# Kernel tuning notes

Measured on AMD Instinct MI355X. Metric: run time of the kernel, lower is better.

The kernel has to match this reference:

```python
import jax, jax.numpy as jnp
import numpy as np


def _conv2d_same(x, w):
    # x: [B,Cin,H,W], w: [Cout,Cin,3,3], stride 1, padding 1
    return jax.lax.conv_general_dilated(
        x, w, window_strides=(1, 1), padding=[(1, 1), (1, 1)],
        dimension_numbers=('NCHW', 'OIHW', 'NCHW'))


def _unfold3x3(x):
    # torch.nn.Unfold(kernel_size=3, padding=1, stride=1):
    # output [B, C*9, H*W], channel-major then kernel row-major ordering.
    b, c, h, w = x.shape
    xp = jnp.pad(x, ((0, 0), (0, 0), (1, 1), (1, 1)))
    patches = jnp.stack(
        [xp[:, :, i:i + h, j:j + w] for i in range(3) for j in range(3)],
        axis=2)  # [B, C, 9, H, W]
    return patches.reshape(b, c * 9, h * w)


def setup_inputs() -> dict:
    key = jax.random.key(0)
    ks = jax.random.split(key, 6)
    B, C, H, W = 16, 64, 128, 128
    R = 16
    return {
        'x': jax.random.normal(ks[0], (B, C, H, W), dtype=jnp.float32),
        'weight': jax.random.normal(ks[1], (C, C, 3, 3), dtype=jnp.float32) * 0.1,
        'se_w1': jax.random.normal(ks[2], (16, C, 3, 3), dtype=jnp.float32) * 0.1,
        'se_w2': jax.random.normal(ks[3], (1, 16, 3, 3), dtype=jnp.float32) * 0.1,
        'fc_w1': jax.random.normal(ks[4], (C // R, C), dtype=jnp.float32) * 0.1,
        'fc_w2': jax.random.normal(ks[5], (9 * C, C // R), dtype=jnp.float32) * 0.1,
    }


def reference(x, weight, se_w1, se_w2, fc_w1, fc_w2):
    b, c, h, w = x.shape
    # channel attention: global avg pool -> fc -> sigmoid, y: [B, C*9]
    y = x.mean(axis=(2, 3))                                   # [B, C]
    y = jax.nn.relu(y @ fc_w1.T)                              # [B, C//r]
    y = jax.nn.sigmoid(y @ fc_w2.T)                           # [B, 9C]
    # spatial attention A: [B, 1, H, W]
    A = jax.nn.sigmoid(_conv2d_same(jax.nn.relu(_conv2d_same(x, se_w1)), se_w2))
    out_unfold = _unfold3x3(x)                                # [B, C*9, HW]
    out_unfold = out_unfold * A.reshape(b, 1, h * w) * y[:, :, None]
    wf = weight.reshape(c, c * 9)                             # [Cout, C*9]
    out = jnp.einsum('bkl,ok->bol', out_unfold, wf)           # [B, Cout, HW]
    return out.reshape(b, c, h, w)
```

## Files before the change

### kernel.cpp

```cpp
#include <hip/hip_runtime.h>
#include <hip/hip_bf16.h>
#include <math.h>

#define B_  16
#define C_  64
#define H_  128
#define W_  128
#define HW_ (H_ * W_)
#define CR_ 4
#define K9C (9 * C_)
#define TW  130
#define FBS 36
#define STG_W 36
#define STG_H 12
#define MIDOFF (STG_H * STG_W * 128)
#define MIDS 18
#define WTB 8192
#define W2OFF (MIDOFF + 3 * WTB)
#define LDSZ  (W2OFF + 144 * 4)

typedef float f32x4 __attribute__((ext_vector_type(4)));
typedef __bf16 bf16x8 __attribute__((ext_vector_type(8)));

static __device__ __forceinline__ unsigned short f2us(float f) {
    __bf16 h = (__bf16)f;
    return __builtin_bit_cast(unsigned short, h);
}

static __device__ __forceinline__ int swz64(int blk) {
    int xcd = blk & 7, i = blk >> 3;
    return ((i >> 6) << 9) + (xcd << 6) + (i & 63);
}

__global__ void k_tr(const float* __restrict__ x, unsigned short* __restrict__ t,
                     float* __restrict__ y0p) {
    int blk = blockIdx.x;
    int b = blk >> 7, y = blk & 127;
    __shared__ unsigned short lds[C_ * TW];
    int tid = threadIdx.x;
    for (int i = tid; i < C_ * 32; i += 256) {
        int c = i >> 5, xq = i & 31;
        float4 v = *(const float4*)(x + (((size_t)(b * C_ + c)) << 14) + (y << 7) + (xq << 2));
        unsigned int p0 = f2us(v.x) | ((unsigned int)f2us(v.y) << 16);
        unsigned int p1 = f2us(v.z) | ((unsigned int)f2us(v.w) << 16);
        *(unsigned int*)&lds[c * TW + (xq << 2)]     = p0;
        *(unsigned int*)&lds[c * TW + (xq << 2) + 2] = p1;
        float s4 = v.x + v.y + v.z + v.w;
        s4 += __shfl_down(s4, 16, 32);
        s4 += __shfl_down(s4, 8, 32);
        s4 += __shfl_down(s4, 4, 32);
        s4 += __shfl_down(s4, 2, 32);
        s4 += __shfl_down(s4, 1, 32);
        if ((tid & 31) == 0) y0p[(((b << 7) + y) << 6) + c] = s4;
    }
    __syncthreads();
    size_t rowbase = ((size_t)(b * TW + y + 1)) * TW * C_;
    for (int j = tid; j < 128 * 16; j += 256) {
        int px = j >> 4, g = j & 15;
        unsigned short a0 = lds[(4 * g + 0) * TW + px];
        unsigned short a1 = lds[(4 * g + 1) * TW + px];
        unsigned short a2 = lds[(4 * g + 2) * TW + px];
        unsigned short a3 = lds[(4 * g + 3) * TW + px];
        uint2 wv;
        wv.x = a0 | ((unsigned int)a1 << 16);
        wv.y = a2 | ((unsigned int)a3 << 16);
        *(uint2*)(t + rowbase + (size_t)(px + 1) * C_ + (g << 2)) = wv;
    }
    if (tid < 16) {
        int px = (tid < 8) ? 0 : (TW - 1);
        int ch = tid & 7;
        uint4 z = {0, 0, 0, 0};
        *(uint4*)(t + rowbase + (size_t)px * C_ + ch * 8) = z;
    }
    if (y == 0) {
        size_t base = (size_t)b * TW * TW * C_;
        uint4 z = {0, 0, 0, 0};
        for (int i = tid; i < TW * C_ / 8; i += 256)
            *(uint4*)(t + base + (size_t)i * 8) = z;
    }
    if (y == 127) {
        size_t base = ((size_t)(b * TW + TW - 1)) * TW * C_;
        uint4 z = {0, 0, 0, 0};
        for (int i = tid; i < TW * C_ / 8; i += 256)
            *(uint4*)(t + base + (size_t)i * 8) = z;
    }
}

__global__ void k_attwt(const float* __restrict__ y0p,
                        const float* __restrict__ fc_w1,
                        const float* __restrict__ fc_w2,
                        const float* __restrict__ weight,
                        const float* __restrict__ se_w1,
                        unsigned short* __restrict__ w_t,
                        unsigned short* __restrict__ w1t) {
    int blk = blockIdx.x;
    int b = blk >> 2, mt = blk & 3;
    __shared__ float sy0[C_];
    __shared__ float sh[CR_];
    __shared__ float ssy[K9C];
    __shared__ float sw[16 * 576];
    int tid = threadIdx.x;
    if (blk == 0) {
        for (int i = tid; i < 9 * 16 * C_; i += 256) {
            int tap = i >> 10, o = (i >> 6) & 15, c = i & 63;
            w1t[i] = f2us(se_w1[(o * C_ + c) * 9 + tap]);
        }
    }
    if (tid < C_) {
        float s = 0.f;
        const float* pp = y0p + ((size_t)b << 13) + tid;
        for (int y = 0; y < 128; ++y) s += pp[y << 6];
        sy0[tid] = s * (1.0f / (float)HW_);
    }
    const float* wsrc = weight + (size_t)(mt * 16) * 576;
    for (int i = tid; i < 16 * 576; i += 256) sw[i] = wsrc[i];
    __syncthreads();
    if (tid < CR_) {
        float s = 0.f;
        for (int c = 0; c < C_; ++c) s = fmaf(fc_w1[tid * C_ + c], sy0[c], s);
        sh[tid] = fmaxf(s, 0.f);
    }
    __syncthreads();
    for (int i = tid; i < K9C; i += 256) {
        float s = 0.f;
        #pragma unroll
        for (int j = 0; j < CR_; ++j) s = fmaf(fc_w2[i * CR_ + j], sh[j], s);
        ssy[i] = 1.f / (1.f + expf(-s));
    }
    __syncthreads();
    unsigned short* wb = w_t + (size_t)b * 9 * C_ * C_;
    for (int ii = tid; ii < 4608; ii += 256) {
        int i = ii << 1;
        int tap = i >> 10, r = i & 1023;
        int half = r >> 9, lane = (r >> 3) & 63, e = r & 7;
        int o = lane & 15;
        int c = half * 32 + ((lane >> 4) << 3) + e;
        float v0 = sw[o * 576 + c * 9 + tap] * ssy[c * 9 + tap];
        float v1 = sw[o * 576 + (c + 1) * 9 + tap] * ssy[(c + 1) * 9 + tap];
        unsigned int pk = f2us(v0) | ((unsigned int)f2us(v1) << 16);
        *(unsigned int*)(wb + ((tap * 4 + mt) * 2 + half) * 512 + lane * 8 + e) = pk;
    }
}

__global__ void __launch_bounds__(512, 4)
k_fused(const unsigned short* __restrict__ t, const unsigned short* __restrict__ w_t,
        const unsigned short* __restrict__ w1t, const float* __restrict__ se_w2,
        float* __restrict__ out) {
    int blk = swz64(blockIdx.x);
    int b = blk >> 6, tile = blk & 63;
    int ty0 = (tile >> 2) << 3, tx0 = (tile & 3) << 5;
    int tid = threadIdx.x, lane = tid & 63, wave = tid >> 6;
    int wy = wave >> 1, wx = wave & 1;
    int n = lane & 15, q = lane >> 4, qc = q << 3;
    __shared__ __align__(16) char smem[LDSZ];
    float* fb  = (float*)smem;
    float* mid = (float*)(smem + MIDOFF);
    float* w2l = (float*)(smem + W2OFF);

    const unsigned short* tbb = t + (size_t)b * TW * TW * C_;
    #pragma unroll
    for (int it = 0; it < 7; ++it) {
        int s = (it << 9) + tid;
        if (s < STG_H * STG_W * 8) {
            int row = s / 288, r = s % 288, px = r >> 3, chp = r & 7;
            int tr = ty0 - 1 + row; tr = tr < 0 ? 0 : (tr > TW - 1 ? TW - 1 : tr);
            int tc = tx0 - 1 + px;  tc = tc < 0 ? 0 : (tc > TW - 1 ? TW - 1 : tc);
            int ch = chp ^ (px & 7);
            __builtin_amdgcn_global_load_lds(
                (const __attribute__((address_space(1))) void*)(tbb + ((size_t)tr * TW + tc) * C_ + (ch << 3)),
                (__attribute__((address_space(3))) void*)(smem + (s << 4)), 16, 0, 0);
        }
    }
    if (tid < 144) w2l[tid] = se_w2[(tid & 15) * 9 + (tid >> 4)];

    const unsigned short* wb = w_t + (size_t)b * 9 * C_ * C_;
    #define STAGE_WT(tp) \
        __builtin_amdgcn_global_load_lds( \
            (const __attribute__((address_space(1))) void*)(wb + (tp) * 4096 + (wave << 9) + (lane << 3)), \
            (__attribute__((address_space(3))) void*)(smem + MIDOFF + ((tp) % 3) * WTB + (wave << 10)), \
            16, 0, 0)
    STAGE_WT(0);
    STAGE_WT(1);
    __syncthreads();

    f32x4 acc[4][2] = {};
    #pragma unroll
    for (int tap = 0; tap < 9; ++tap) {
        if (tap) {
            if (tap < 8) asm volatile("s_waitcnt vmcnt(1)" ::: "memory");
            else         asm volatile("s_waitcnt vmcnt(0)" ::: "memory");
            __builtin_amdgcn_s_barrier();
            __builtin_amdgcn_sched_barrier(0);
        }
        if (tap < 7) STAGE_WT(tap + 2);
        int ki = tap / 3, kj = tap % 3;
        int xl = (wx << 4) + n + kj + 1;
        int xk = xl & 7;
        const char* tapbuf = smem + MIDOFF + (tap % 3) * WTB;
        __builtin_amdgcn_s_setprio(1);
        #pragma unroll
        for (int half = 0; half < 2; ++half) {
            bf16x8 af[4];
            #pragma unroll
            for (int mt = 0; mt < 4; ++mt) {
                uint4 au = *(const uint4*)(tapbuf + (((mt << 1) + half) << 10) + (lane << 4));
                af[mt] = __builtin_bit_cast(bf16x8, au);
            }
            int slot = (((half << 2) + q) ^ xk) << 4;
            #pragma unroll
            for (int j2 = 0; j2 < 2; ++j2) {
                int yl = (wy << 1) + j2 + ki + 1;
                bf16x8 bf = *(const bf16x8*)(smem + (yl * STG_W + xl) * 128 + slot);
                #pragma unroll
                for (int mt = 0; mt < 4; ++mt)
                    acc[mt][j2] = __builtin_amdgcn_mfma_f32_16x16x32_bf16(af[mt], bf, acc[mt][j2], 0, 0, 0);
            }
        }
        __builtin_amdgcn_s_setprio(0);
    }
    #undef STAGE_WT
    __syncthreads();

    int mr[3], mc[3], pp[3];
    bool on[3];
    #pragma unroll
    for (int i = 0; i < 3; ++i) {
        int g = wave + (i << 3);
        on[i] = (g < 22);
        int p = g * 16 + n; if (p > 339) p = 339;
        pp[i] = p; mr[i] = p / 34; mc[i] = p - mr[i] * 34;
    }
    f32x4 a1_0 = {}, a1_1 = {}, a1_2 = {};
    __builtin_amdgcn_s_setprio(1);
    #pragma unroll
    for (int tap = 0; tap < 9; ++tap) {
        int ki = tap / 3, kj = tap % 3;
        uint4 u0 = *(const uint4*)(w1t + (tap * 16 + n) * C_ + qc);
        uint4 u1 = *(const uint4*)(w1t + (tap * 16 + n) * C_ + 32 + qc);
        bf16x8 af0 = __builtin_bit_cast(bf16x8, u0);
        bf16x8 af1 = __builtin_bit_cast(bf16x8, u1);
        #pragma unroll
        for (int i = 0; i < 3; ++i) {
            if (on[i]) {
                int sc = mc[i] + kj;
                int sb = ((mr[i] + ki) * STG_W + sc) * 128;
                bf16x8 b0 = *(const bf16x8*)(smem + sb + ((q ^ (sc & 7)) << 4));
                bf16x8 b1 = *(const bf16x8*)(smem + sb + (((4 + q) ^ (sc & 7)) << 4));
                f32x4 t0 = (i == 0) ? a1_0 : (i == 1) ? a1_1 : a1_2;
                t0 = __builtin_amdgcn_mfma_f32_16x16x32_bf16(af0, b0, t0, 0, 0, 0);
                t0 = __builtin_amdgcn_mfma_f32_16x16x32_bf16(af1, b1, t0, 0, 0, 0);
                if (i == 0) a1_0 = t0; else if (i == 1) a1_1 = t0; else a1_2 = t0;
            }
        }
    }
    __builtin_amdgcn_s_setprio(0);
    #pragma unroll
    for (int i = 0; i < 3; ++i) {
        int g = wave + (i << 3);
        if (on[i] && (g < 21 || n < 4)) {
            int my = ty0 - 1 + mr[i], mx = tx0 - 1 + mc[i];
            bool valid = (my >= 0) && (my < 128) && (mx >= 0) && (mx < 128);
            f32x4 av = (i == 0) ? a1_0 : (i == 1) ? a1_1 : a1_2;
            #pragma unroll
            for (int r = 0; r < 4; ++r)
                mid[pp[i] * MIDS + (q << 2) + r] = valid ? fmaxf(av[r], 0.f) : 0.f;
        }
    }
    __syncthreads();

    float4 wq[9];
    #pragma unroll
    for (int tap = 0; tap < 9; ++tap)
        wq[tap] = *(const float4*)&w2l[tap * 16 + (q << 2)];
    float Av[2];
    #pragma unroll
    for (int j2 = 0; j2 < 2; ++j2) {
        float s = 0.f;
        #pragma unroll
        for (int di = 0; di < 3; ++di) {
            #pragma unroll
            for (int dj = 0; dj < 3; ++dj) {
                int p = ((wy << 1) + j2 + di) * 34 + (wx << 4) + n + dj;
                const float* mp = &mid[p * MIDS + (q << 2)];
                float2 m0 = *(const float2*)mp;
                float2 m1 = *(const float2*)(mp + 2);
                float4 wv = wq[di * 3 + dj];
                s = fmaf(m0.x, wv.x, s);
                s = fmaf(m0.y, wv.y, s);
                s = fmaf(m1.x, wv.z, s);
                s = fmaf(m1.y, wv.w, s);
            }
        }
        s += __shfl_xor(s, 16, 64);
        s += __shfl_xor(s, 32, 64);
        Av[j2] = 1.f / (1.f + expf(-s));
    }

    __syncthreads();
    #pragma unroll
    for (int j2 = 0; j2 < 2; ++j2) {
        #pragma unroll
        for (int mt = 0; mt < 4; ++mt) {
            #pragma unroll
            for (int r = 0; r < 4; ++r) {
                int o = (mt << 4) + (q << 2) + r;
                fb[((j2 << 8) + (wy << 6) + o) * FBS + (wx << 4) + n] = acc[mt][j2][r] * Av[j2];
            }
        }
    }
    __syncthreads();
    #pragma unroll
    for (int it = 0; it < 8; ++it) {
        int s = it * 512 + tid;
        int row = s >> 3, xq = s & 7;
        int j2 = row >> 8, rr = row & 255;
        int wy2 = rr >> 6, o = rr & 63;
        float4 v = *(const float4*)&fb[row * FBS + (xq << 2)];
        *(float4*)(out + (((size_t)(b * C_ + o)) << 14) +
                   ((ty0 + (wy2 << 1) + j2) << 7) + tx0 + (xq << 2)) = v;
    }
}

extern "C" void kernel_launch(void* const* d_in, const int* in_sizes, int n_in,
                              void* d_out, int out_size, void* d_ws, size_t ws_size,
                              hipStream_t stream) {
    const float* x      = (const float*)d_in[0];
    const float* weight = (const float*)d_in[1];
    const float* se_w1  = (const float*)d_in[2];
    const float* se_w2  = (const float*)d_in[3];
    const float* fc_w1  = (const float*)d_in[4];
    const float* fc_w2  = (const float*)d_in[5];
    float* out = (float*)d_out;

    char* ws = (char*)d_ws;
    float* y0p           = (float*)ws;                         ws += (size_t)B_ * H_ * C_ * 4;
    unsigned short* t    = (unsigned short*)ws;                ws += (size_t)B_ * TW * TW * C_ * 2 + 4096;
    unsigned short* w_t  = (unsigned short*)ws;                ws += (size_t)B_ * 9 * C_ * C_ * 2;
    unsigned short* w1t  = (unsigned short*)ws;

    k_tr   <<<B_ * H_, 256, 0, stream>>>(x, t, y0p);
    k_attwt<<<B_ * 4, 256, 0, stream>>>(y0p, fc_w1, fc_w2, weight, se_w1, w_t, w1t);
    k_fused<<<B_ * 64, 512, 0, stream>>>(t, w_t, w1t, se_w2, out);
}
```

Baseline: 175.3 us.

## Pack channel pairs in transpose LDS with XOR swizzle and split attention-weight kernel

The transpose kernel now loads two channels per thread and packs them into 32-bit words in a swizzled LDS tile. This replaces four 16-bit strided reads per output with two 32-bit reads, cutting bank conflicts and LDS instruction count. The attention/weight-prep kernel goes from 64 to 256 blocks: the mean reduction is spread across all threads and the per-tap weight packing is divided into four chunks. Each extra block redundantly recomputes the small FC/sigmoid stage in exchange for more parallelism in this short kernel.

```diff
diff --git a/kernel.cpp b/kernel.cpp
--- a/kernel.cpp
+++ b/kernel.cpp
@@ -36,35 +36,44 @@
                      float* __restrict__ y0p) {
     int blk = blockIdx.x;
     int b = blk >> 7, y = blk & 127;
-    __shared__ unsigned short lds[C_ * TW];
+    __shared__ unsigned int lds2[32 * 128];
     int tid = threadIdx.x;
-    for (int i = tid; i < C_ * 32; i += 256) {
-        int c = i >> 5, xq = i & 31;
-        float4 v = *(const float4*)(x + (((size_t)(b * C_ + c)) << 14) + (y << 7) + (xq << 2));
-        unsigned int p0 = f2us(v.x) | ((unsigned int)f2us(v.y) << 16);
-        unsigned int p1 = f2us(v.z) | ((unsigned int)f2us(v.w) << 16);
-        *(unsigned int*)&lds[c * TW + (xq << 2)]     = p0;
-        *(unsigned int*)&lds[c * TW + (xq << 2) + 2] = p1;
-        float s4 = v.x + v.y + v.z + v.w;
-        s4 += __shfl_down(s4, 16, 32);
-        s4 += __shfl_down(s4, 8, 32);
-        s4 += __shfl_down(s4, 4, 32);
-        s4 += __shfl_down(s4, 2, 32);
-        s4 += __shfl_down(s4, 1, 32);
-        if ((tid & 31) == 0) y0p[(((b << 7) + y) << 6) + c] = s4;
+    int cpair = tid >> 3, q8 = tid & 7;
+    int F = (cpair & 15) << 1;
+    const float* x0 = x + (((size_t)(b * C_ + (cpair << 1))) << 14) + (y << 7);
+    float s0 = 0.f, s1 = 0.f;
+    #pragma unroll
+    for (int k = 0; k < 4; ++k) {
+        int px0 = (q8 + (k << 3)) << 2;
+        float4 v0 = *(const float4*)(x0 + px0);
+        float4 v1 = *(const float4*)(x0 + 16384 + px0);
+        s0 += v0.x + v0.y + v0.z + v0.w;
+        s1 += v1.x + v1.y + v1.z + v1.w;
+        uint2 a, c;
+        a.x = f2us(v0.x) | ((unsigned int)f2us(v1.x) << 16);
+        a.y = f2us(v0.y) | ((unsigned int)f2us(v1.y) << 16);
+        c.x = f2us(v0.z) | ((unsigned int)f2us(v1.z) << 16);
+        c.y = f2us(v0.w) | ((unsigned int)f2us(v1.w) << 16);
+        *(uint2*)&lds2[(cpair << 7) + (px0 ^ F)] = a;
+        *(uint2*)&lds2[(cpair << 7) + ((px0 + 2) ^ F)] = c;
+    }
+    s0 += __shfl_down(s0, 4, 8); s0 += __shfl_down(s0, 2, 8); s0 += __shfl_down(s0, 1, 8);
+    s1 += __shfl_down(s1, 4, 8); s1 += __shfl_down(s1, 2, 8); s1 += __shfl_down(s1, 1, 8);
+    if (q8 == 0) {
+        float2 m = {s0, s1};
+        *(float2*)&y0p[(((b << 7) + y) << 6) + (cpair << 1)] = m;
     }
     __syncthreads();
     size_t rowbase = ((size_t)(b * TW + y + 1)) * TW * C_;
-    for (int j = tid; j < 128 * 16; j += 256) {
-        int px = j >> 4, g = j & 15;
-        unsigned short a0 = lds[(4 * g + 0) * TW + px];
-        unsigned short a1 = lds[(4 * g + 1) * TW + px];
-        unsigned short a2 = lds[(4 * g + 2) * TW + px];
-        unsigned short a3 = lds[(4 * g + 3) * TW + px];
+    #pragma unroll
+    for (int k = 0; k < 8; ++k) {
+        int j = tid + (k << 8);
+        int px = j >> 4, gq = j & 15;
+        int r0 = gq << 1, r1 = r0 + 1;
         uint2 wv;
-        wv.x = a0 | ((unsigned int)a1 << 16);
-        wv.y = a2 | ((unsigned int)a3 << 16);
-        *(uint2*)(t + rowbase + (size_t)(px + 1) * C_ + (g << 2)) = wv;
+        wv.x = lds2[(r0 << 7) + (px ^ ((r0 & 15) << 1))];
+        wv.y = lds2[(r1 << 7) + (px ^ ((r1 & 15) << 1))];
+        *(uint2*)(t + rowbase + (size_t)(px + 1) * C_ + (gq << 2)) = wv;
     }
     if (tid < 16) {
         int px = (tid < 8) ? 0 : (TW - 1);
@@ -94,26 +103,31 @@
                         unsigned short* __restrict__ w_t,
                         unsigned short* __restrict__ w1t) {
     int blk = blockIdx.x;
-    int b = blk >> 2, mt = blk & 3;
+    int b = blk >> 4, part = blk & 15, mt = part >> 2, hk = part & 3;
+    __shared__ float red[256];
     __shared__ float sy0[C_];
     __shared__ float sh[CR_];
     __shared__ float ssy[K9C];
     __shared__ float sw[16 * 576];
     int tid = threadIdx.x;
-    if (blk == 0) {
-        for (int i = tid; i < 9 * 16 * C_; i += 256) {
-            int tap = i >> 10, o = (i >> 6) & 15, c = i & 63;
-            w1t[i] = f2us(se_w1[(o * C_ + c) * 9 + tap]);
-        }
-    }
-    if (tid < C_) {
+    if (b == 0 && part < 9) {
+        int tap = part;
+        for (int j = tid; j < 1024; j += 256)
+            w1t[tap * 1024 + j] = f2us(se_w1[j * 9 + tap]);
+    }
+    {
         float s = 0.f;
-        const float* pp = y0p + ((size_t)b << 13) + tid;
-        for (int y = 0; y < 128; ++y) s += pp[y << 6];
-        sy0[tid] = s * (1.0f / (float)HW_);
+        const float* pp = y0p + ((size_t)b << 13) + ((tid >> 6) << 11) + (tid & 63);
+        #pragma unroll
+        for (int yy = 0; yy < 32; ++yy) s += pp[yy << 6];
+        red[tid] = s;
     }
     const float* wsrc = weight + (size_t)(mt * 16) * 576;
     for (int i = tid; i < 16 * 576; i += 256) sw[i] = wsrc[i];
+    __syncthreads();
+    if (tid < C_)
+        sy0[tid] = (red[tid] + red[tid + 64] + red[tid + 128] + red[tid + 192])
+                   * (1.0f / (float)HW_);
     __syncthreads();
     if (tid < CR_) {
         float s = 0.f;
@@ -129,7 +143,7 @@
     }
     __syncthreads();
     unsigned short* wb = w_t + (size_t)b * 9 * C_ * C_;
-    for (int ii = tid; ii < 4608; ii += 256) {
+    for (int ii = hk * 1152 + tid; ii < (hk + 1) * 1152; ii += 256) {
         int i = ii << 1;
         int tap = i >> 10, r = i & 1023;
         int half = r >> 9, lane = (r >> 3) & 63, e = r & 7;
@@ -339,6 +353,6 @@
     unsigned short* w1t  = (unsigned short*)ws;
 
     k_tr   <<<B_ * H_, 256, 0, stream>>>(x, t, y0p);
-    k_attwt<<<B_ * 4, 256, 0, stream>>>(y0p, fc_w1, fc_w2, weight, se_w1, w_t, w1t);
+    k_attwt<<<B_ * 16, 256, 0, stream>>>(y0p, fc_w1, fc_w2, weight, se_w1, w_t, w1t);
     k_fused<<<B_ * 64, 512, 0, stream>>>(t, w_t, w1t, se_w2, out);
 }
```

Result: faster. 169.2 us (-3.5%).
